# Kernel tuning notes

Hardware: AMD Instinct MI355X
Metric: run time of the kernel (lower is better)

## Reference

```python
import jax, jax.numpy as jnp
import numpy as np

H = 4096
B = 64


def _lstm_cell(x, h, c, W_ih, W_hh, b_ih, b_hh):
    # PyTorch gate order: i, f, g, o. gates: [B, 4H]
    gates = x @ W_ih.T + b_ih + h @ W_hh.T + b_hh
    i, f, g, o = jnp.split(gates, 4, axis=-1)
    c_new = jax.nn.sigmoid(f) * c + jax.nn.sigmoid(i) * jnp.tanh(g)
    h_new = jax.nn.sigmoid(o) * jnp.tanh(c_new)
    return h_new, c_new


def setup_inputs() -> dict:
    key = jax.random.key(0)
    ks = jax.random.split(key, 16)
    s = 0.02
    inp = {
        "current_features": jax.random.normal(ks[0], (B, H), jnp.float32),
        "h0": jax.random.normal(ks[1], (2, B, H), jnp.float32),
        "c0": jax.random.normal(ks[2], (2, B, H), jnp.float32),
        # LSTM layer 0
        "W_ih0": jax.random.normal(ks[3], (4 * H, H), jnp.float32) * s,
        "W_hh0": jax.random.normal(ks[4], (4 * H, H), jnp.float32) * s,
        "b_ih0": jax.random.normal(ks[5], (4 * H,), jnp.float32) * s,
        "b_hh0": jax.random.normal(ks[6], (4 * H,), jnp.float32) * s,
        # LSTM layer 1
        "W_ih1": jax.random.normal(ks[7], (4 * H, H), jnp.float32) * s,
        "W_hh1": jax.random.normal(ks[8], (4 * H, H), jnp.float32) * s,
        "b_ih1": jax.random.normal(ks[9], (4 * H,), jnp.float32) * s,
        "b_hh1": jax.random.normal(ks[10], (4 * H,), jnp.float32) * s,
        # count estimator head
        "Wc1": jax.random.normal(ks[11], (H // 2, H), jnp.float32) * s,
        "bc1": jax.random.normal(ks[12], (H // 2,), jnp.float32) * s,
        "Wc2": jax.random.normal(ks[13], (1, H // 2), jnp.float32) * s,
        "bc2": jax.random.normal(ks[14], (1,), jnp.float32) * s,
    }
    return inp


def reference(current_features, h0, c0,
              W_ih0, W_hh0, b_ih0, b_hh0,
              W_ih1, W_hh1, b_ih1, b_hh1,
              Wc1, bc1, Wc2, bc2):
    # Single-step 2-layer LSTM (seq_len=1; inter-layer dropout inactive in eval)
    h1, c1 = _lstm_cell(current_features, h0[0], c0[0], W_ih0, W_hh0, b_ih0, b_hh0)
    h2, c2 = _lstm_cell(h1, h0[1], c0[1], W_ih1, W_hh1, b_ih1, b_hh1)
    memory_state = h2  # [B, H]
    h_new = jnp.stack([h1, h2], axis=0)  # [2, B, H]
    c_new = jnp.stack([c1, c2], axis=0)
    # count head: Linear -> ReLU -> Linear -> ReLU
    hid = jax.nn.relu(memory_state @ Wc1.T + bc1)
    count_estimate = jax.nn.relu(hid @ Wc2.T + bc2)  # [B, 1]
    return memory_state, (h_new, c_new), count_estimate
```

## Files before the change

### kernel.cpp

```cpp
#include <hip/hip_runtime.h>

#define HD 4096

typedef __attribute__((ext_vector_type(4))) float f32x4;
typedef __attribute__((ext_vector_type(8))) short bf16x8;
typedef __attribute__((ext_vector_type(4))) short s16x4;
typedef __attribute__((ext_vector_type(2))) unsigned u32x2;

__device__ __forceinline__ short f2bf(float f) {
    unsigned u = __float_as_uint(f);
    u += 0x7fffu + ((u >> 16) & 1u);
    return (short)(u >> 16);
}

__device__ __forceinline__ float sigmoidf_(float x) { return 1.f / (1.f + __expf(-x)); }

__global__ void convert_kernel(const float* __restrict__ X, const float* __restrict__ h0,
                               short* __restrict__ Xbf, short* __restrict__ H0bf)
{
    const int i = blockIdx.x * blockDim.x + threadIdx.x;
    if (i < 65536) {
        f32x4 v = ((const f32x4*)X)[i];
        s16x4 o = { f2bf(v[0]), f2bf(v[1]), f2bf(v[2]), f2bf(v[3]) };
        ((s16x4*)Xbf)[i] = o;
    } else {
        const int j = i - 65536;
        f32x4 v = ((const f32x4*)h0)[j];
        s16x4 o = { f2bf(v[0]), f2bf(v[1]), f2bf(v[2]), f2bf(v[3]) };
        ((s16x4*)H0bf)[j] = o;
    }
}

#define ISSUE(TP) do { \
    const float* gp_ = gw + (long)(TP) * 256; \
    _Pragma("unroll") for (int r_ = 0; r_ < 16; ++r_) \
        sreg[r_] = *(const f32x4*)(gp_ + r_ * HD); \
    __builtin_amdgcn_sched_barrier(0); \
} while (0)

#define CVTWRITE(BUF) do { \
    char* lb_ = (char*)&wlds[wv][(BUF)][0]; \
    _Pragma("unroll") for (int r_ = 0; r_ < 16; ++r_) { \
        unsigned lo_, hi_; \
        asm("v_cvt_pk_bf16_f32 %0, %1, %2" : "=v"(lo_) : "v"(sreg[r_][0]), "v"(sreg[r_][1])); \
        asm("v_cvt_pk_bf16_f32 %0, %1, %2" : "=v"(hi_) : "v"(sreg[r_][2]), "v"(sreg[r_][3])); \
        u32x2 v_ = { lo_, hi_ }; \
        *(u32x2*)(lb_ + r_ * 512 + (((lane >> 1) ^ (r_ & 7)) << 4) + ((lane & 1) << 3)) = v_; \
    } \
} while (0)

#define COMPUTE(TP, BUF) do { \
    const short* ab_ = aBase + (long)(TP) * 256; \
    const char* lr_ = (const char*)&wlds[wv][(BUF)][0] + ar * 512; \
    _Pragma("unroll") for (int ks_ = 0; ks_ < 8; ++ks_) { \
        const int g_ = (ks_ * 4 + kg) ^ (ar & 7); \
        const bf16x8 b_ = *(const bf16x8*)(lr_ + g_ * 16); \
        _Pragma("unroll") for (int m_ = 0; m_ < 4; ++m_) { \
            const bf16x8 a_ = *(const bf16x8*)(ab_ + m_ * 16 * HD + ks_ * 32); \
            acc[m_] = __builtin_amdgcn_mfma_f32_16x16x32_bf16(a_, b_, acc[m_], 0, 0, 0); \
        } \
    } \
} while (0)

__global__ __launch_bounds__(256, 2) void gemm_part_kernel(
    const short* __restrict__ A0, const short* __restrict__ A1,
    const float* __restrict__ W0, const float* __restrict__ W1,
    float* __restrict__ P, int N, int nkq, int KB)
{
    __shared__ short wlds[4][2][4096];
    const int tid = threadIdx.x, lane = tid & 63, wv = tid >> 6;
    const int ar = lane & 15, kg = lane >> 4;
    const int bid = blockIdx.x;
    const int ntile = bid / nkq, kq = bid % nkq;
    const int half = nkq >> 1;
    const int kqh = (kq >= half) ? 1 : 0;
    const int kqi = kq - kqh * half;
    const short* A = kqh ? A1 : A0;
    const float* W = kqh ? W1 : W0;
    const int kbase = kqi * KB;
    const int T = KB >> 8;
    const int phase = (bid + wv * (T >> 2)) & (T - 1);
    const int n0w = ntile * 64 + wv * 16;

    const float* gw = W + (long)n0w * HD + kbase + lane * 4;
    const short* aBase = A + (long)ar * HD + kbase + kg * 8;

    const f32x4 zero = {0.f, 0.f, 0.f, 0.f};
    f32x4 acc[4] = {zero, zero, zero, zero};
    f32x4 sreg[16];

    ISSUE(phase);
    asm volatile("s_waitcnt vmcnt(0)" ::: "memory");
    __builtin_amdgcn_sched_barrier(0);
    CVTWRITE(0);
    if (T > 1) ISSUE((1 + phase) & (T - 1));
    asm volatile("s_waitcnt lgkmcnt(0)" ::: "memory");
    __builtin_amdgcn_sched_barrier(0);

    for (int t = 0; t < T; ++t) {
        const int tp = (t + phase) & (T - 1);
        COMPUTE(tp, t & 1);
        if (t + 1 < T) {
            asm volatile("s_waitcnt vmcnt(0)" ::: "memory");
            __builtin_amdgcn_sched_barrier(0);
            CVTWRITE((t + 1) & 1);
            if (t + 2 < T) ISSUE((t + 2 + phase) & (T - 1));
            asm volatile("s_waitcnt lgkmcnt(0)" ::: "memory");
            __builtin_amdgcn_sched_barrier(0);
        }
    }

    float* pr = P + (long)kq * 64 * N + n0w + ar;
    #pragma unroll
    for (int m = 0; m < 4; ++m)
        #pragma unroll
        for (int r = 0; r < 4; ++r)
            pr[(long)(m * 16 + kg * 4 + r) * N] = acc[m][r];
}

__global__ void cell_kernel(const float* __restrict__ P, int nkq,
                            const float* __restrict__ bi, const float* __restrict__ bh,
                            const float* __restrict__ cprev,
                            float* __restrict__ hout, float* __restrict__ cout,
                            float* __restrict__ ms, short* __restrict__ hbf)
{
    const int idx = blockIdx.x * blockDim.x + threadIdx.x;
    const int b = idx >> 10;
    const int hc = (idx & 1023) * 4;

    f32x4 g[4] = {{0,0,0,0},{0,0,0,0},{0,0,0,0},{0,0,0,0}};
    for (int kq = 0; kq < nkq; ++kq) {
        const float* pb = P + ((long)kq * 64 + b) * 16384 + hc;
        #pragma unroll
        for (int gt = 0; gt < 4; ++gt)
            g[gt] += *(const f32x4*)(pb + gt * 4096);
    }
    #pragma unroll
    for (int gt = 0; gt < 4; ++gt) {
        g[gt] += *(const f32x4*)(bi + gt * HD + hc);
        g[gt] += *(const f32x4*)(bh + gt * HD + hc);
    }
    const long off = (long)b * HD + hc;
    f32x4 c = *(const f32x4*)(cprev + off);
    f32x4 hn, cn; s16x4 hb;
    #pragma unroll
    for (int e = 0; e < 4; ++e) {
        float cv = sigmoidf_(g[1][e]) * c[e] + sigmoidf_(g[0][e]) * tanhf(g[2][e]);
        float hv = sigmoidf_(g[3][e]) * tanhf(cv);
        cn[e] = cv; hn[e] = hv; hb[e] = f2bf(hv);
    }
    *(f32x4*)(hout + off) = hn;
    *(f32x4*)(cout + off) = cn;
    if (ms) *(f32x4*)(ms + off) = hn;
    *(s16x4*)(hbf + off) = hb;
}

__global__ void headfin_kernel(const float* __restrict__ P, int nkq,
                               const float* __restrict__ bc1, float* __restrict__ hid)
{
    const int idx = blockIdx.x * blockDim.x + threadIdx.x;
    const int b = idx >> 9;
    const int n = (idx & 511) * 4;
    f32x4 s = {0.f, 0.f, 0.f, 0.f};
    for (int kq = 0; kq < nkq; ++kq)
        s += *(const f32x4*)(P + ((long)kq * 64 + b) * 2048 + n);
    s += *(const f32x4*)(bc1 + n);
    #pragma unroll
    for (int e = 0; e < 4; ++e) s[e] = fmaxf(s[e], 0.f);
    *(f32x4*)(hid + (long)b * 2048 + n) = s;
}

__global__ void count_kernel(const float* __restrict__ hid, const float* __restrict__ Wc2,
                             const float* __restrict__ bc2, float* __restrict__ out)
{
    const int tid = threadIdx.x;
    const int b = tid >> 2, q = tid & 3;
    const float* hp = hid + (long)b * 2048 + q * 512;
    const float* wp = Wc2 + q * 512;
    float s = 0.f;
    #pragma unroll 4
    for (int k = 0; k < 512; k += 4) {
        f32x4 h4 = *(const f32x4*)(hp + k);
        f32x4 w4 = *(const f32x4*)(wp + k);
        s += h4[0] * w4[0] + h4[1] * w4[1] + h4[2] * w4[2] + h4[3] * w4[3];
    }
    s += __shfl_xor(s, 1);
    s += __shfl_xor(s, 2);
    if (q == 0) out[b] = fmaxf(s + bc2[0], 0.f);
}

extern "C" void kernel_launch(void* const* d_in, const int* in_sizes, int n_in,
                              void* d_out, int out_size, void* d_ws, size_t ws_size,
                              hipStream_t stream)
{
    const float* X    = (const float*)d_in[0];
    const float* h0   = (const float*)d_in[1];
    const float* c0   = (const float*)d_in[2];
    const float* Wih0 = (const float*)d_in[3];
    const float* Whh0 = (const float*)d_in[4];
    const float* bih0 = (const float*)d_in[5];
    const float* bhh0 = (const float*)d_in[6];
    const float* Wih1 = (const float*)d_in[7];
    const float* Whh1 = (const float*)d_in[8];
    const float* bih1 = (const float*)d_in[9];
    const float* bhh1 = (const float*)d_in[10];
    const float* Wc1  = (const float*)d_in[11];
    const float* bc1  = (const float*)d_in[12];
    const float* Wc2  = (const float*)d_in[13];
    const float* bc2  = (const float*)d_in[14];

    float* out  = (float*)d_out;
    float* ms   = out;
    float* hnew = out + 262144;
    float* cnew = out + 786432;
    float* cnt  = out + 1310720;

    char* ws = (char*)d_ws;
    short* Xbf  = (short*)ws;
    short* H0bf = (short*)(ws + (1u << 19));
    short* h1bf = (short*)(ws + 3u * (1u << 19));
    short* h2bf = (short*)(ws + (1u << 21));
    float* hid  = (float*)(ws + 5u * (1u << 19));
    float* Pp   = (float*)(ws + 3u * (1u << 20));

    hipLaunchKernelGGL(convert_kernel, dim3(768), dim3(256), 0, stream, X, h0, Xbf, H0bf);

    hipLaunchKernelGGL(gemm_part_kernel, dim3(512), dim3(256), 0, stream,
                       Xbf, H0bf, Wih0, Whh0, Pp, 16384, 2, 4096);
    hipLaunchKernelGGL(cell_kernel, dim3(256), dim3(256), 0, stream,
                       Pp, 2, bih0, bhh0, c0, hnew, cnew, (float*)nullptr, h1bf);

    hipLaunchKernelGGL(gemm_part_kernel, dim3(512), dim3(256), 0, stream,
                       h1bf, H0bf + 262144, Wih1, Whh1, Pp, 16384, 2, 4096);
    hipLaunchKernelGGL(cell_kernel, dim3(256), dim3(256), 0, stream,
                       Pp, 2, bih1, bhh1, c0 + 262144, hnew + 262144, cnew + 262144, ms, h2bf);

    hipLaunchKernelGGL(gemm_part_kernel, dim3(256), dim3(256), 0, stream,
                       h2bf, h2bf + 2048, Wc1, Wc1 + 2048, Pp, 2048, 8, 512);
    hipLaunchKernelGGL(headfin_kernel, dim3(128), dim3(256), 0, stream, Pp, 8, bc1, hid);
    hipLaunchKernelGGL(count_kernel, dim3(1), dim3(256), 0, stream, hid, Wc2, bc2, cnt);
}
```

Before: 405.1 us.

## Replace split-K GEMM with small panel GEMM and bf16 partial sums

Swaps the 64-column, 2-way split-K GEMM for a panel kernel. Each 128-thread block loads a 16-row by 1024-K slice of fp32 weights, converts it to bf16 in LDS, then multiplies it by the batch activations with MFMA. The grid grows to 8192 blocks per LSTM layer and the K split grows to 8 partials, which are stored as bf16 to halve partial-sum traffic. The goal is more parallelism and better latency hiding on the weight stream, which is what bounds this workload. In exchange it adds more partial-sum reduction work and some precision loss from rounding the partial sums to bf16.

```diff
diff --git a/kernel.cpp b/kernel.cpp
--- a/kernel.cpp
+++ b/kernel.cpp
@@ -12,7 +12,9 @@
     u += 0x7fffu + ((u >> 16) & 1u);
     return (short)(u >> 16);
 }
-
+__device__ __forceinline__ float bf2f(short s) {
+    return __uint_as_float(((unsigned)(unsigned short)s) << 16);
+}
 __device__ __forceinline__ float sigmoidf_(float x) { return 1.f / (1.f + __expf(-x)); }
 
 __global__ void convert_kernel(const float* __restrict__ X, const float* __restrict__ h0,
@@ -31,94 +33,96 @@
     }
 }
 
-#define ISSUE(TP) do { \
-    const float* gp_ = gw + (long)(TP) * 256; \
-    _Pragma("unroll") for (int r_ = 0; r_ < 16; ++r_) \
-        sreg[r_] = *(const f32x4*)(gp_ + r_ * HD); \
-    __builtin_amdgcn_sched_barrier(0); \
-} while (0)
-
-#define CVTWRITE(BUF) do { \
-    char* lb_ = (char*)&wlds[wv][(BUF)][0]; \
-    _Pragma("unroll") for (int r_ = 0; r_ < 16; ++r_) { \
-        unsigned lo_, hi_; \
-        asm("v_cvt_pk_bf16_f32 %0, %1, %2" : "=v"(lo_) : "v"(sreg[r_][0]), "v"(sreg[r_][1])); \
-        asm("v_cvt_pk_bf16_f32 %0, %1, %2" : "=v"(hi_) : "v"(sreg[r_][2]), "v"(sreg[r_][3])); \
-        u32x2 v_ = { lo_, hi_ }; \
-        *(u32x2*)(lb_ + r_ * 512 + (((lane >> 1) ^ (r_ & 7)) << 4) + ((lane & 1) << 3)) = v_; \
-    } \
-} while (0)
-
-#define COMPUTE(TP, BUF) do { \
-    const short* ab_ = aBase + (long)(TP) * 256; \
-    const char* lr_ = (const char*)&wlds[wv][(BUF)][0] + ar * 512; \
-    _Pragma("unroll") for (int ks_ = 0; ks_ < 8; ++ks_) { \
-        const int g_ = (ks_ * 4 + kg) ^ (ar & 7); \
-        const bf16x8 b_ = *(const bf16x8*)(lr_ + g_ * 16); \
-        _Pragma("unroll") for (int m_ = 0; m_ < 4; ++m_) { \
-            const bf16x8 a_ = *(const bf16x8*)(ab_ + m_ * 16 * HD + ks_ * 32); \
-            acc[m_] = __builtin_amdgcn_mfma_f32_16x16x32_bf16(a_, b_, acc[m_], 0, 0, 0); \
-        } \
-    } \
-} while (0)
-
-__global__ __launch_bounds__(256, 2) void gemm_part_kernel(
+__global__ __launch_bounds__(128, 2) void panel_gemm_kernel(
     const short* __restrict__ A0, const short* __restrict__ A1,
     const float* __restrict__ W0, const float* __restrict__ W1,
-    float* __restrict__ P, int N, int nkq, int KB)
-{
-    __shared__ short wlds[4][2][4096];
+    short* __restrict__ P, int Ntot, int npan)
+{
+    __shared__ short smem[16][1024];
     const int tid = threadIdx.x, lane = tid & 63, wv = tid >> 6;
     const int ar = lane & 15, kg = lane >> 4;
     const int bid = blockIdx.x;
-    const int ntile = bid / nkq, kq = bid % nkq;
-    const int half = nkq >> 1;
-    const int kqh = (kq >= half) ? 1 : 0;
-    const int kqi = kq - kqh * half;
-    const short* A = kqh ? A1 : A0;
-    const float* W = kqh ? W1 : W0;
-    const int kbase = kqi * KB;
-    const int T = KB >> 8;
-    const int phase = (bid + wv * (T >> 2)) & (T - 1);
-    const int n0w = ntile * 64 + wv * 16;
-
-    const float* gw = W + (long)n0w * HD + kbase + lane * 4;
-    const short* aBase = A + (long)ar * HD + kbase + kg * 8;
-
-    const f32x4 zero = {0.f, 0.f, 0.f, 0.f};
-    f32x4 acc[4] = {zero, zero, zero, zero};
-    f32x4 sreg[16];
-
-    ISSUE(phase);
-    asm volatile("s_waitcnt vmcnt(0)" ::: "memory");
-    __builtin_amdgcn_sched_barrier(0);
-    CVTWRITE(0);
-    if (T > 1) ISSUE((1 + phase) & (T - 1));
-    asm volatile("s_waitcnt lgkmcnt(0)" ::: "memory");
-    __builtin_amdgcn_sched_barrier(0);
-
-    for (int t = 0; t < T; ++t) {
-        const int tp = (t + phase) & (T - 1);
-        COMPUTE(tp, t & 1);
-        if (t + 1 < T) {
-            asm volatile("s_waitcnt vmcnt(0)" ::: "memory");
-            __builtin_amdgcn_sched_barrier(0);
-            CVTWRITE((t + 1) & 1);
-            if (t + 2 < T) ISSUE((t + 2 + phase) & (T - 1));
-            asm volatile("s_waitcnt lgkmcnt(0)" ::: "memory");
-            __builtin_amdgcn_sched_barrier(0);
+    const int group = npan * 4;
+    const int mat = bid / group;
+    const int rem = bid - mat * group;
+    const int p = rem >> 2, khq = rem & 3;
+    const short* A = mat ? A1 : A0;
+    const float* W = mat ? W1 : W0;
+    const int kq = mat * 4 + khq;
+    const int n0 = p * 16;
+
+    const float* wb = W + (long)n0 * HD + khq * 1024 + (lane << 2);
+    char* lds = (char*)&smem[0][0];
+    f32x4 rr[2][4];
+
+#define ISSUE_ROW(RQ, RR) do { \
+    const float* rp_ = wb + (long)(wv * 8 + (RR)) * HD; \
+    _Pragma("unroll") for (int j_ = 0; j_ < 4; ++j_) \
+        rr[RQ][j_] = *(const f32x4*)(rp_ + j_ * 256); \
+    __builtin_amdgcn_sched_barrier(0); \
+} while (0)
+
+    ISSUE_ROW(0, 0);
+    ISSUE_ROW(1, 1);
+    #pragma unroll
+    for (int r = 0; r < 8; ++r) {
+        const int R = wv * 8 + r;
+        const int q = r & 1;
+        char* rowb = lds + R * 2048 + ((lane & 1) << 3);
+        #pragma unroll
+        for (int j = 0; j < 4; ++j) {
+            unsigned lo_, hi_;
+            asm("v_cvt_pk_bf16_f32 %0, %1, %2" : "=v"(lo_) : "v"(rr[q][j][0]), "v"(rr[q][j][1]));
+            asm("v_cvt_pk_bf16_f32 %0, %1, %2" : "=v"(hi_) : "v"(rr[q][j][2]), "v"(rr[q][j][3]));
+            const int g = (j * 32 + (lane >> 1)) ^ (R & 7);
+            u32x2 v_ = { lo_, hi_ };
+            *(u32x2*)(rowb + g * 16) = v_;
         }
-    }
-
-    float* pr = P + (long)kq * 64 * N + n0w + ar;
-    #pragma unroll
-    for (int m = 0; m < 4; ++m)
-        #pragma unroll
-        for (int r = 0; r < 4; ++r)
-            pr[(long)(m * 16 + kg * 4 + r) * N] = acc[m][r];
-}
-
-__global__ void cell_kernel(const float* __restrict__ P, int nkq,
+        if (r + 2 < 8) ISSUE_ROW(q, r + 2);
+    }
+    __syncthreads();
+
+    const short* ab = A + (long)(wv * 32 + ar) * HD + khq * 1024 + kg * 8;
+    const char* lb = lds + ar * 2048;
+    const int swz = ar & 7;
+
+    f32x4 acc0 = {0.f, 0.f, 0.f, 0.f}, acc1 = {0.f, 0.f, 0.f, 0.f};
+    bf16x8 aR[4][2];
+    bf16x8 bR[2];
+
+    #pragma unroll
+    for (int s = 0; s < 4; ++s) {
+        aR[s][0] = *(const bf16x8*)(ab + s * 32);
+        aR[s][1] = *(const bf16x8*)(ab + 65536 + s * 32);
+    }
+    bR[0] = *(const bf16x8*)(lb + (((kg) ^ swz) << 4));
+    bR[1] = *(const bf16x8*)(lb + (((4 + kg) ^ swz) << 4));
+
+    for (int su = 0; su < 8; ++su) {
+        #pragma unroll
+        for (int i = 0; i < 4; ++i) {
+            const int s = su * 4 + i;
+            acc0 = __builtin_amdgcn_mfma_f32_16x16x32_bf16(aR[i][0], bR[i & 1], acc0, 0, 0, 0);
+            acc1 = __builtin_amdgcn_mfma_f32_16x16x32_bf16(aR[i][1], bR[i & 1], acc1, 0, 0, 0);
+            if (su < 7) {
+                aR[i][0] = *(const bf16x8*)(ab + (s + 4) * 32);
+                aR[i][1] = *(const bf16x8*)(ab + 65536 + (s + 4) * 32);
+            }
+            if (su < 7 || i < 2) {
+                bR[i & 1] = *(const bf16x8*)(lb + ((((s + 2) * 4 + kg) ^ swz) << 4));
+            }
+        }
+    }
+
+    short* pr = P + ((long)kq * 64 + wv * 32) * Ntot + n0 + ar;
+    #pragma unroll
+    for (int r = 0; r < 4; ++r) {
+        pr[(long)(kg * 4 + r) * Ntot]      = f2bf(acc0[r]);
+        pr[(long)(16 + kg * 4 + r) * Ntot] = f2bf(acc1[r]);
+    }
+}
+
+__global__ void cell_kernel(const short* __restrict__ P, int nkq,
                             const float* __restrict__ bi, const float* __restrict__ bh,
                             const float* __restrict__ cprev,
                             float* __restrict__ hout, float* __restrict__ cout,
@@ -130,10 +134,13 @@
 
     f32x4 g[4] = {{0,0,0,0},{0,0,0,0},{0,0,0,0},{0,0,0,0}};
     for (int kq = 0; kq < nkq; ++kq) {
-        const float* pb = P + ((long)kq * 64 + b) * 16384 + hc;
-        #pragma unroll
-        for (int gt = 0; gt < 4; ++gt)
-            g[gt] += *(const f32x4*)(pb + gt * 4096);
+        const short* pb = P + ((long)kq * 64 + b) * 16384 + hc;
+        #pragma unroll
+        for (int gt = 0; gt < 4; ++gt) {
+            s16x4 v = *(const s16x4*)(pb + gt * 4096);
+            #pragma unroll
+            for (int e = 0; e < 4; ++e) g[gt][e] += bf2f(v[e]);
+        }
     }
     #pragma unroll
     for (int gt = 0; gt < 4; ++gt) {
@@ -155,15 +162,18 @@
     *(s16x4*)(hbf + off) = hb;
 }
 
-__global__ void headfin_kernel(const float* __restrict__ P, int nkq,
+__global__ void headfin_kernel(const short* __restrict__ P, int nkq,
                                const float* __restrict__ bc1, float* __restrict__ hid)
 {
     const int idx = blockIdx.x * blockDim.x + threadIdx.x;
     const int b = idx >> 9;
     const int n = (idx & 511) * 4;
     f32x4 s = {0.f, 0.f, 0.f, 0.f};
-    for (int kq = 0; kq < nkq; ++kq)
-        s += *(const f32x4*)(P + ((long)kq * 64 + b) * 2048 + n);
+    for (int kq = 0; kq < nkq; ++kq) {
+        s16x4 v = *(const s16x4*)(P + ((long)kq * 64 + b) * 2048 + n);
+        #pragma unroll
+        for (int e = 0; e < 4; ++e) s[e] += bf2f(v[e]);
+    }
     s += *(const f32x4*)(bc1 + n);
     #pragma unroll
     for (int e = 0; e < 4; ++e) s[e] = fmaxf(s[e], 0.f);
@@ -221,22 +231,22 @@
     short* h1bf = (short*)(ws + 3u * (1u << 19));
     short* h2bf = (short*)(ws + (1u << 21));
     float* hid  = (float*)(ws + 5u * (1u << 19));
-    float* Pp   = (float*)(ws + 3u * (1u << 20));
+    short* Pp   = (short*)(ws + 3u * (1u << 20));
 
     hipLaunchKernelGGL(convert_kernel, dim3(768), dim3(256), 0, stream, X, h0, Xbf, H0bf);
 
-    hipLaunchKernelGGL(gemm_part_kernel, dim3(512), dim3(256), 0, stream,
-                       Xbf, H0bf, Wih0, Whh0, Pp, 16384, 2, 4096);
+    hipLaunchKernelGGL(panel_gemm_kernel, dim3(8192), dim3(128), 0, stream,
+                       Xbf, H0bf, Wih0, Whh0, Pp, 16384, 1024);
     hipLaunchKernelGGL(cell_kernel, dim3(256), dim3(256), 0, stream,
-                       Pp, 2, bih0, bhh0, c0, hnew, cnew, (float*)nullptr, h1bf);
-
-    hipLaunchKernelGGL(gemm_part_kernel, dim3(512), dim3(256), 0, stream,
-                       h1bf, H0bf + 262144, Wih1, Whh1, Pp, 16384, 2, 4096);
+                       Pp, 8, bih0, bhh0, c0, hnew, cnew, (float*)nullptr, h1bf);
+
+    hipLaunchKernelGGL(panel_gemm_kernel, dim3(8192), dim3(128), 0, stream,
+                       h1bf, H0bf + 262144, Wih1, Whh1, Pp, 16384, 1024);
     hipLaunchKernelGGL(cell_kernel, dim3(256), dim3(256), 0, stream,
-                       Pp, 2, bih1, bhh1, c0 + 262144, hnew + 262144, cnew + 262144, ms, h2bf);
-
-    hipLaunchKernelGGL(gemm_part_kernel, dim3(256), dim3(256), 0, stream,
-                       h2bf, h2bf + 2048, Wc1, Wc1 + 2048, Pp, 2048, 8, 512);
-    hipLaunchKernelGGL(headfin_kernel, dim3(128), dim3(256), 0, stream, Pp, 8, bc1, hid);
+                       Pp, 8, bih1, bhh1, c0 + 262144, hnew + 262144, cnew + 262144, ms, h2bf);
+
+    hipLaunchKernelGGL(panel_gemm_kernel, dim3(512), dim3(128), 0, stream,
+                       h2bf, h2bf, Wc1, Wc1, Pp, 2048, 128);
+    hipLaunchKernelGGL(headfin_kernel, dim3(128), dim3(256), 0, stream, Pp, 4, bc1, hid);
     hipLaunchKernelGGL(count_kernel, dim3(1), dim3(256), 0, stream, hid, Wc2, bc2, cnt);
 }
```

Result: slower. 430.9 us (+6.4%).
